# Performance work log

Measured on AMD Instinct MI355X. Metric: run time of the kernel, lower is better.

## Reference

```python
import jax, jax.numpy as jnp
import numpy as np

B, D, H, W, K = 2, 128, 256, 256, 4
OFFSET_SCALE = 1.0
BN_EPS = 1e-5


def conv2d(x, w, b=None, pad='SAME'):
    y = jax.lax.conv_general_dilated(x, w, (1, 1), pad,
                                     dimension_numbers=('NCHW', 'OIHW', 'NCHW'))
    if b is not None:
        y = y + b[None, :, None, None]
    return y


def grid_sample_border(img, gx, gy):
    # img: (b,d,H,W); gx,gy: (b,K,H,W) normalized coords in [-1,1]
    # bilinear, padding_mode='border', align_corners=True
    b, d, h, w = img.shape
    x = jnp.clip((gx + 1.0) * 0.5 * (w - 1), 0.0, w - 1)
    y = jnp.clip((gy + 1.0) * 0.5 * (h - 1), 0.0, h - 1)
    x0f = jnp.floor(x); y0f = jnp.floor(y)
    wx = x - x0f; wy = y - y0f
    x0 = x0f.astype(jnp.int32); y0 = y0f.astype(jnp.int32)
    x1 = jnp.minimum(x0 + 1, w - 1); y1 = jnp.minimum(y0 + 1, h - 1)
    imgT = jnp.transpose(img, (0, 2, 3, 1))  # (b,H,W,d)
    bidx = jnp.arange(b)[:, None, None, None]  # broadcasts over (b,K,H,W)
    def gather(yi, xi):
        return imgT[bidx, yi, xi]  # (b,K,H,W,d)
    out = (gather(y0, x0) * ((1 - wx) * (1 - wy))[..., None]
           + gather(y0, x1) * (wx * (1 - wy))[..., None]
           + gather(y1, x0) * ((1 - wx) * wy)[..., None]
           + gather(y1, x1) * (wx * wy)[..., None])
    return out  # (b,K,H,W,d)


def setup_inputs() -> dict:
    key = jax.random.key(0)
    ks = jax.random.split(key, 6)
    return {
        'bev': jax.random.normal(ks[0], (B, D, H, W), jnp.float32),
        'offset_w': jax.random.normal(ks[1], (2 * K, D, 3, 3), jnp.float32) * 0.02,
        'offset_b': jax.random.normal(ks[2], (2 * K,), jnp.float32) * 0.02,
        'weight_w': jax.random.normal(ks[3], (K, D, 3, 3), jnp.float32) * 0.05,
        'weight_b': jnp.zeros((K,), jnp.float32),
        'proj_w': jax.random.normal(ks[4], (D, D, 1, 1), jnp.float32) * (1.0 / np.sqrt(D)),
        'bn_gamma': jnp.ones((D,), jnp.float32),
        'bn_beta': jnp.zeros((D,), jnp.float32),
    }


def reference(bev, offset_w, offset_b, weight_w, weight_b, proj_w, bn_gamma, bn_beta):
    b, d, h, w = bev.shape
    # per-pixel K offsets (pixels) and K attention weights
    offsets = conv2d(bev, offset_w, offset_b) * OFFSET_SCALE  # (b,2K,H,W)
    w_logits = conv2d(bev, weight_w, weight_b)                # (b,K,H,W)
    attn = jax.nn.softmax(w_logits, axis=1)                   # softmax over K
    # base grid: replicates torch meshgrid(xy) + transpose (requires H==W)
    xs = jnp.linspace(-1.0, 1.0, w)
    ys = jnp.linspace(-1.0, 1.0, h)
    base_x = xs[:, None] * jnp.ones((1, h), jnp.float32)  # base_x[i,j] = xs[i]
    base_y = jnp.ones((w, 1), jnp.float32) * ys[None, :]  # base_y[i,j] = ys[j]
    off = offsets.reshape(b, K, 2, h, w)
    dx = off[:, :, 0]  # (b,K,H,W)
    dy = off[:, :, 1]
    dx_n = dx * (2.0 / (w - 1)) if w > 1 else dx * 0.0
    dy_n = dy * (2.0 / (h - 1)) if h > 1 else dy * 0.0
    gx = base_x[None, None] + dx_n  # (b,K,H,W)
    gy = base_y[None, None] + dy_n
    sampled = grid_sample_border(bev, gx, gy)  # (b,K,H,W,d)
    aggregated = jnp.einsum('bkhwd,bkhw->bdhw', sampled, attn)
    # proj: 1x1 conv (no bias) + BatchNorm2d (training mode: batch stats) + GELU(exact)
    y = conv2d(aggregated, proj_w)
    mean = jnp.mean(y, axis=(0, 2, 3), keepdims=True)
    var = jnp.mean((y - mean) ** 2, axis=(0, 2, 3), keepdims=True)
    y = (y - mean) * jax.lax.rsqrt(var + BN_EPS)
    y = y * bn_gamma[None, :, None, None] + bn_beta[None, :, None, None]
    return jax.nn.gelu(y, approximate=False)
```

## Files before the change

### kernel.cpp

```cpp
#include <hip/hip_runtime.h>
#include <math.h>

#define BB 2
#define DD 128
#define HH 256
#define WW 256
#define KK 4
#define HWC (HH*WW)
#define SROW2 320

typedef unsigned int u32;
typedef unsigned short ushort;
typedef __attribute__((ext_vector_type(8))) short bf16x8;
typedef __attribute__((ext_vector_type(4))) float f32x4;

#define OA_OFF    0
#define WTT_OFF   1572864
#define WP_OFF    1589248
#define STATS_OFF 1603072
#define PART_OFF  1603392
#define BEVT_OFF  1605440
#define YBF_OFF   9994048
#define PACC_OFF  18382656
#define PART2_OFF PACC_OFF
#define WBF_OFF   26771264
#define WCB_OFF   26779456
#define WS_NEED_BEVT  ((size_t)PACC_OFF * 4)
#define WS_NEED_FULL3 ((size_t)(WCB_OFF + 9216) * 4)

__device__ __forceinline__ u32 f2bf(float x) {
    u32 u = __builtin_bit_cast(u32, x);
    return (u + 0x7fffu + ((u >> 16) & 1u)) >> 16;
}
__device__ __forceinline__ u32 pkbf(float a, float b) {
    return f2bf(a) | (f2bf(b) << 16);
}
__device__ __forceinline__ float bflo(u32 d) { return __builtin_bit_cast(float, d << 16); }
__device__ __forceinline__ float bfhi(u32 d) { return __builtin_bit_cast(float, d & 0xffff0000u); }

__global__ __launch_bounds__(256) void k0_prep(
    const float* __restrict__ projw, const float* __restrict__ offw,
    const float* __restrict__ wtw, float* __restrict__ wtT, float* __restrict__ wp)
{
    int idx = blockIdx.x * 256 + threadIdx.x;
    if (idx < 16384) {
        int d = idx >> 7, o = idx & 127;
        wtT[d * 128 + o] = projw[o * 128 + d];
    }
    if (idx < 13824) {
        int c = idx / 108; int r = idx % 108; int o = r / 9; int t = r % 9;
        wp[idx] = (o < 8) ? offw[(o*128 + c)*9 + t] : wtw[((o-8)*128 + c)*9 + t];
    }
}

__global__ __launch_bounds__(256) void k0bc(
    const float* __restrict__ projw, const float* __restrict__ offw,
    const float* __restrict__ wtw, ushort* __restrict__ wbf,
    ushort* __restrict__ wcb)
{
    int idx = blockIdx.x * 256 + threadIdx.x;
    if (idx < 16384) wbf[idx] = (ushort)f2bf(projw[idx]);
    if (idx < 18432) {
        int tap = idx >> 11;
        int rem = idx & 2047;
        int oo = rem >> 7, c = rem & 127;
        float v = 0.f;
        if (oo < 8)       v = offw[(oo*128 + c)*9 + tap];
        else if (oo < 12) v = wtw[((oo-8)*128 + c)*9 + tap];
        wcb[idx] = (ushort)f2bf(v);
    }
}

__global__ __launch_bounds__(256) void k2t_bf(
    const float* __restrict__ bev, ushort* __restrict__ bevtb)
{
    __shared__ float T[64 * 128];
    int tid = threadIdx.x;
    int bidx = blockIdx.x;
    int b = bidx >> 10;
    int rem = bidx & 1023;
    int yrow = rem >> 2;
    int x0 = (rem & 3) << 6;

    const float* src = bev + ((size_t)b * DD) * HWC + (size_t)yrow * WW + x0;
    #pragma unroll 4
    for (int k = 0; k < 32; k++) {
        int flat = k * 256 + tid;
        int d = flat >> 6, xl = flat & 63;
        float v = src[(size_t)d * HWC + xl];
        T[xl * 128 + (((d >> 2) ^ (xl & 31)) << 2) + (d & 3)] = v;
    }
    __syncthreads();
    ushort* dst = bevtb + (((size_t)b * HH + yrow) * WW + x0) * 128;
    #pragma unroll 4
    for (int k = 0; k < 8; k++) {
        int flat = k * 256 + tid;
        int d4 = flat & 31, xl = (flat >> 5) & 63;
        float4 v = *(const float4*)&T[xl * 128 + ((d4 ^ (xl & 31)) << 2)];
        uint2 pk;
        pk.x = pkbf(v.x, v.y);
        pk.y = pkbf(v.z, v.w);
        *(uint2*)(dst + (size_t)xl * 128 + (d4 << 2)) = pk;
    }
}

__global__ __launch_bounds__(256) void k1m_conv_mfma(
    const ushort* __restrict__ bevtb, const ushort* __restrict__ wcb,
    const float* __restrict__ offb, const float* __restrict__ wtb,
    float* __restrict__ oa)
{
    __shared__ uint4 lds4[3168];

    int tid = threadIdx.x;
    int wv = tid >> 6;
    int l = tid & 63;
    int lm = l & 15, lk = l >> 4;
    int wgid = blockIdx.x;
    int lin = (wgid & 7) * 256 + (wgid >> 3);
    int b = lin >> 10;
    int i = (lin >> 2) & 255;
    int jt = lin & 3;
    int x0 = jt * 64;

    const ushort* bb = bevtb + (size_t)b * HWC * 128;
    for (int z = tid; z < 3168; z += 256) {
        int row = z / 1056;
        int rem = z - row * 1056;
        int pl = rem >> 4;
        int q  = rem & 15;
        int yy = i - 1 + row;
        int x  = x0 - 1 + pl;
        bool ok = ((unsigned)yy < HH) && ((unsigned)x < WW);
        uint4 v = make_uint4(0u, 0u, 0u, 0u);
        if (ok) v = *(const uint4*)(bb + ((size_t)(yy * WW + x) << 7) + q * 8);
        lds4[row * 1056 + pl * 16 + (q ^ (pl & 15))] = v;
    }
    __syncthreads();

    f32x4 acc = (f32x4)(0.f);
    #pragma unroll
    for (int dy = 0; dy < 3; dy++) {
        #pragma unroll
        for (int dx = 0; dx < 3; dx++) {
            int pl = wv * 16 + lm + dx;
            const uint4* bp = &lds4[dy * 1056 + pl * 16];
            int sx = pl & 15;
            const ushort* ap = wcb + (size_t)((dy*3 + dx) * 16 + lm) * 128 + lk * 8;
            #pragma unroll
            for (int kk = 0; kk < 4; kk++) {
                bf16x8 bfr = *(const bf16x8*)&bp[(kk*4 + lk) ^ sx];
                bf16x8 afr = *(const bf16x8*)(ap + kk * 32);
                acc = __builtin_amdgcn_mfma_f32_16x16x32_bf16(afr, bfr, acc, 0, 0, 0);
            }
        }
    }

    float v[4];
    #pragma unroll
    for (int r = 0; r < 4; r++) v[r] = acc[r];

    int j = x0 + wv * 16 + lm;
    if (lk < 2) {
        #pragma unroll
        for (int r = 0; r < 4; r++) v[r] += offb[lk*4 + r];
    } else if (lk == 2) {
        float l4[4];
        #pragma unroll
        for (int r = 0; r < 4; r++) l4[r] = v[r] + wtb[r];
        float m = fmaxf(fmaxf(l4[0], l4[1]), fmaxf(l4[2], l4[3]));
        float e[4]; float se = 0.f;
        #pragma unroll
        for (int r = 0; r < 4; r++) { e[r] = expf(l4[r] - m); se += e[r]; }
        float inv = 1.f / se;
        #pragma unroll
        for (int r = 0; r < 4; r++) v[r] = e[r] * inv;
    }
    if (lk < 3) {
        size_t basep = (size_t)b * 12 * HWC + (size_t)i * WW + j;
        #pragma unroll
        for (int r = 0; r < 4; r++)
            oa[basep + (size_t)(lk*4 + r) * HWC] = v[r];
    }
}

#define TAPPTR(t) (bt + ((size_t)((((t) & 1) ? (pa[(t) >> 1] >> 16) : (pa[(t) >> 1] & 0xffffu))) << 7))
#define FMA8(S, V, W) do { \
    S[0] = fmaf(W, bflo((V).x), S[0]); S[1] = fmaf(W, bfhi((V).x), S[1]); \
    S[2] = fmaf(W, bflo((V).y), S[2]); S[3] = fmaf(W, bfhi((V).y), S[3]); \
    S[4] = fmaf(W, bflo((V).z), S[4]); S[5] = fmaf(W, bfhi((V).z), S[5]); \
    S[6] = fmaf(W, bflo((V).w), S[6]); S[7] = fmaf(W, bfhi((V).w), S[7]); \
} while (0)

__global__ __launch_bounds__(256, 4) void k2f_sample_proj(
    const ushort* __restrict__ bevtb, const float* __restrict__ oa,
    const ushort* __restrict__ wbf, ushort* __restrict__ ybf,
    float* __restrict__ part2)
{
    __shared__ uint4 P[32 * 16];

    int tid = threadIdx.x;
    int wgid = blockIdx.x;
    int lin = (wgid & 7) * 512 + (wgid >> 3);
    int b = lin >> 11;
    int pix0 = (lin & 2047) << 5;

    int q8 = tid & 7;
    int pixl = tid >> 3;
    int pix = pix0 + pixl;
    int p = pix >> 8;
    int q = pix & 255;

    const float* ob = oa + (size_t)b * 12 * HWC + (size_t)p * WW + q;
    unsigned pa[8]; float cw[16];
    #pragma unroll
    for (int k = 0; k < 4; k++) {
        float dx = ob[(size_t)(2*k)   * HWC];
        float dy = ob[(size_t)(2*k+1) * HWC];
        float a  = ob[(size_t)(8+k)   * HWC];
        float x  = fminf(fmaxf((float)p + dx, 0.f), (float)(WW-1));
        float yv = fminf(fmaxf((float)q + dy, 0.f), (float)(HH-1));
        float x0f = floorf(x); float y0f = floorf(yv);
        int x0 = (int)x0f; int y0 = (int)y0f;
        int x1 = min(x0 + 1, WW - 1); int y1 = min(y0 + 1, HH - 1);
        float wx = x - x0f; float wy = yv - y0f;
        pa[k*2+0] = (unsigned)(y0*WW + x0) | ((unsigned)(y0*WW + x1) << 16);
        pa[k*2+1] = (unsigned)(y1*WW + x0) | ((unsigned)(y1*WW + x1) << 16);
        cw[k*4+0] = a * (1.f - wx) * (1.f - wy);
        cw[k*4+1] = a * wx * (1.f - wy);
        cw[k*4+2] = a * (1.f - wx) * wy;
        cw[k*4+3] = a * wx * wy;
    }

    const ushort* bt = bevtb + (size_t)b * HWC * 128 + q8 * 8;

    float s[2][8];
    #pragma unroll
    for (int c = 0; c < 2; c++)
        #pragma unroll
        for (int e = 0; e < 8; e++) s[c][e] = 0.f;

    uint4 L0[8], L1[8];
    #pragma unroll
    for (int t = 0; t < 8; t++) L0[t] = *(const uint4*)(TAPPTR(t));
    #pragma unroll
    for (int t = 0; t < 8; t++) L1[t] = *(const uint4*)(TAPPTR(t + 8));
    #pragma unroll
    for (int t = 0; t < 8; t++) {
        uint4 v = L0[t];
        L0[t] = *(const uint4*)(TAPPTR(t) + 64);
        FMA8(s[0], v, cw[t]);
    }
    #pragma unroll
    for (int t = 0; t < 8; t++) {
        uint4 v = L1[t];
        L1[t] = *(const uint4*)(TAPPTR(t + 8) + 64);
        FMA8(s[0], v, cw[t + 8]);
    }
    #pragma unroll
    for (int t = 0; t < 8; t++) FMA8(s[1], L0[t], cw[t]);
    #pragma unroll
    for (int t = 0; t < 8; t++) FMA8(s[1], L1[t], cw[t + 8]);

    int sxr = pixl & 15;
    #pragma unroll
    for (int c = 0; c < 2; c++) {
        uint4 pk;
        pk.x = pkbf(s[c][0], s[c][1]);
        pk.y = pkbf(s[c][2], s[c][3]);
        pk.z = pkbf(s[c][4], s[c][5]);
        pk.w = pkbf(s[c][6], s[c][7]);
        P[pixl * 16 + ((c * 8 + q8) ^ sxr)] = pk;
    }
    __syncthreads();

    int wv = tid >> 6;
    int l = tid & 63;
    int lm = l & 15, lk = l >> 4;
    int o0 = wv << 5;

    f32x4 acc[2][2];
    #pragma unroll
    for (int ot = 0; ot < 2; ot++)
        #pragma unroll
        for (int nt = 0; nt < 2; nt++)
            acc[ot][nt] = (f32x4)(0.f);

    #pragma unroll
    for (int ot = 0; ot < 2; ot++) {
        const ushort* ap = wbf + (size_t)(o0 + ot * 16 + lm) * 128 + lk * 8;
        bf16x8 a4[4];
        #pragma unroll
        for (int kk = 0; kk < 4; kk++)
            a4[kk] = *(const bf16x8*)(ap + kk * 32);
        #pragma unroll
        for (int nt = 0; nt < 2; nt++) {
            int row = nt * 16 + lm;
            #pragma unroll
            for (int kk = 0; kk < 4; kk++) {
                bf16x8 bfr = *(const bf16x8*)&P[row * 16 + ((kk * 4 + lk) ^ lm)];
                acc[ot][nt] = __builtin_amdgcn_mfma_f32_16x16x32_bf16(
                    a4[kk], bfr, acc[ot][nt], 0, 0, 0);
            }
        }
    }

    #pragma unroll
    for (int ot = 0; ot < 2; ot++)
        #pragma unroll
        for (int nt = 0; nt < 2; nt++)
            #pragma unroll
            for (int r = 0; r < 4; r++)
                ybf[((size_t)b * DD + o0 + ot * 16 + lk * 4 + r) * HWC + pix0 + nt * 16 + lm]
                    = (ushort)f2bf(acc[ot][nt][r]);

    float sm[2][4], sq[2][4];
    #pragma unroll
    for (int ot = 0; ot < 2; ot++)
        #pragma unroll
        for (int r = 0; r < 4; r++) { sm[ot][r] = 0.f; sq[ot][r] = 0.f; }
    #pragma unroll
    for (int ot = 0; ot < 2; ot++)
        #pragma unroll
        for (int nt = 0; nt < 2; nt++)
            #pragma unroll
            for (int r = 0; r < 4; r++) {
                float v = acc[ot][nt][r];
                sm[ot][r] += v;
                sq[ot][r] = fmaf(v, v, sq[ot][r]);
            }
    #pragma unroll
    for (int m = 1; m < 16; m <<= 1) {
        #pragma unroll
        for (int ot = 0; ot < 2; ot++)
            #pragma unroll
            for (int r = 0; r < 4; r++) {
                sm[ot][r] += __shfl_xor(sm[ot][r], m);
                sq[ot][r] += __shfl_xor(sq[ot][r], m);
            }
    }
    if (lm == 0) {
        float* pw = part2 + (size_t)wgid * 256;
        #pragma unroll
        for (int ot = 0; ot < 2; ot++)
            #pragma unroll
            for (int r = 0; r < 4; r++) {
                int o = o0 + ot * 16 + lk * 4 + r;
                pw[o] = sm[ot][r];
                pw[128 + o] = sq[ot][r];
            }
    }
}

__global__ __launch_bounds__(256) void k3b_finalize2(
    const float* __restrict__ part2, const float* __restrict__ gamma,
    const float* __restrict__ beta, float* __restrict__ stats)
{
    int o = blockIdx.x; int tid = threadIdx.x;
    double s = 0.0, s2 = 0.0;
    for (int w = tid; w < 4096; w += 256) {
        s  += (double)part2[(size_t)w * 256 + o];
        s2 += (double)part2[(size_t)w * 256 + 128 + o];
    }
    __shared__ double ls[256], ls2[256];
    ls[tid] = s; ls2[tid] = s2;
    __syncthreads();
    for (int off = 128; off > 0; off >>= 1) {
        if (tid < off) { ls[tid] += ls[tid+off]; ls2[tid] += ls2[tid+off]; }
        __syncthreads();
    }
    if (tid == 0) {
        double N = (double)(BB * HWC);
        double mean = ls[0] / N;
        double var = ls2[0] / N - mean * mean;
        double invs = 1.0 / sqrt(var + 1e-5);
        double g = (double)gamma[o];
        stats[o*2]   = (float)(g * invs);
        stats[o*2+1] = (float)((double)beta[o] - mean * g * invs);
    }
}

__global__ __launch_bounds__(256) void k4_bn_gelu_bf(
    const ushort* __restrict__ ybf, const float* __restrict__ stats,
    float* __restrict__ out)
{
    size_t idx8 = (size_t)blockIdx.x * 256 + threadIdx.x;
    uint4 v = ((const uint4*)ybf)[idx8];
    int o = (int)((idx8 * 8) / HWC) % DD;
    float sc = stats[o*2], sh = stats[o*2+1];
    const float is2 = 0.70710678118654752f;
    float g[8];
    g[0] = fmaf(bflo(v.x), sc, sh); g[1] = fmaf(bfhi(v.x), sc, sh);
    g[2] = fmaf(bflo(v.y), sc, sh); g[3] = fmaf(bfhi(v.y), sc, sh);
    g[4] = fmaf(bflo(v.z), sc, sh); g[5] = fmaf(bfhi(v.z), sc, sh);
    g[6] = fmaf(bflo(v.w), sc, sh); g[7] = fmaf(bfhi(v.w), sc, sh);
    float4 o0, o1;
    o0.x = 0.5f * g[0] * (1.f + erff(g[0] * is2));
    o0.y = 0.5f * g[1] * (1.f + erff(g[1] * is2));
    o0.z = 0.5f * g[2] * (1.f + erff(g[2] * is2));
    o0.w = 0.5f * g[3] * (1.f + erff(g[3] * is2));
    o1.x = 0.5f * g[4] * (1.f + erff(g[4] * is2));
    o1.y = 0.5f * g[5] * (1.f + erff(g[5] * is2));
    o1.z = 0.5f * g[6] * (1.f + erff(g[6] * is2));
    o1.w = 0.5f * g[7] * (1.f + erff(g[7] * is2));
    ((float4*)out)[idx8 * 2]     = o0;
    ((float4*)out)[idx8 * 2 + 1] = o1;
}

__global__ __launch_bounds__(256) void k1_convs(
    const float* __restrict__ bev, const float* __restrict__ wp,
    const float* __restrict__ offb, const float* __restrict__ wtb,
    float* __restrict__ oa)
{
    __shared__ float rows[2][3][260];
    int tid = threadIdx.x;
    int p = blockIdx.x;
    int b = p / HH; int i = p % HH; int j = tid;
    const float* bb = bev + (size_t)b * DD * HWC;

    if (tid < 12) { int bf = tid / 6, r = tid % 6; rows[bf][r >> 1][(r & 1) ? 257 : 0] = 0.f; }
    #pragma unroll
    for (int l = 0; l < 3; l++) {
        int yy = i + l - 1;
        rows[0][l][1 + tid] = ((unsigned)yy < HH) ? bb[yy * WW + tid] : 0.f;
    }
    __syncthreads();

    float acc[12];
    #pragma unroll
    for (int o = 0; o < 12; o++) acc[o] = 0.f;

    for (int c = 0; c < 128; c++) {
        int cb = c & 1, nb = cb ^ 1;
        float rv[3];
        if (c < 127) {
            const float* pln = bb + (size_t)(c + 1) * HWC;
            #pragma unroll
            for (int l = 0; l < 3; l++) {
                int yy = i + l - 1;
                rv[l] = ((unsigned)yy < HH) ? pln[yy * WW + tid] : 0.f;
            }
        }
        float v[9];
        #pragma unroll
        for (int dy = 0; dy < 3; dy++)
            #pragma unroll
            for (int dx = 0; dx < 3; dx++)
                v[dy*3 + dx] = rows[cb][dy][tid + dx];
        const float* wc = wp + c * 108;
        #pragma unroll
        for (int o = 0; o < 12; o++) {
            float s = acc[o];
            #pragma unroll
            for (int t = 0; t < 9; t++) s = fmaf(wc[o*9 + t], v[t], s);
            acc[o] = s;
        }
        if (c < 127) {
            #pragma unroll
            for (int l = 0; l < 3; l++) rows[nb][l][1 + tid] = rv[l];
        }
        __syncthreads();
    }

    float outv[12];
    #pragma unroll
    for (int o = 0; o < 8; o++) outv[o] = acc[o] + offb[o];
    float l4[4];
    #pragma unroll
    for (int k = 0; k < 4; k++) l4[k] = acc[8+k] + wtb[k];
    float m = fmaxf(fmaxf(l4[0], l4[1]), fmaxf(l4[2], l4[3]));
    float e[4]; float se = 0.f;
    #pragma unroll
    for (int k = 0; k < 4; k++) { e[k] = expf(l4[k] - m); se += e[k]; }
    float inv = 1.f / se;
    #pragma unroll
    for (int k = 0; k < 4; k++) outv[8+k] = e[k] * inv;

    size_t basep = (size_t)b * 12 * HWC + (size_t)i * WW + j;
    #pragma unroll
    for (int o = 0; o < 12; o++) oa[basep + (size_t)o * HWC] = outv[o];
}

__global__ __launch_bounds__(512, 2) void k2_sample_proj(
    const float* __restrict__ bev, const float* __restrict__ oa,
    const float* __restrict__ wt, float* __restrict__ y)
{
    __shared__ float S[2][16 * SROW2];
    int tid = threadIdx.x;
    int bidx = blockIdx.x;
    int b  = bidx >> 8;
    int p0 = ((bidx >> 4) & 15) * 16;
    int q0 = (bidx & 15) * 16;
    int pix = tid & 255;
    int gq = pix >> 4;
    int gp = pix & 15;
    int dgrp = tid >> 8;
    int swr = gp * 20 + gq;
    int wv = tid >> 6;
    int wvu = __builtin_amdgcn_readfirstlane(wv);
    int lane = tid & 63;
    int lp = lane >> 2;
    int q4 = (lane & 3) << 2;
    int soff = lp * 20 + q4;

    const float* ob = oa + (size_t)b * 12 * HWC + (size_t)(p0 + gp) * WW + (q0 + gq);
    unsigned pa[8]; float cw[16];
    #pragma unroll
    for (int k = 0; k < 4; k++) {
        float dx = ob[(size_t)(2*k)   * HWC];
        float dy = ob[(size_t)(2*k+1) * HWC];
        float a  = ob[(size_t)(8+k)   * HWC];
        float x  = fminf(fmaxf((float)(p0 + gp) + dx, 0.f), (float)(WW-1));
        float yv = fminf(fmaxf((float)(q0 + gq) + dy, 0.f), (float)(HH-1));
        float x0f = floorf(x); float y0f = floorf(yv);
        int x0 = (int)x0f; int y0 = (int)y0f;
        int x1 = min(x0 + 1, WW - 1); int y1 = min(y0 + 1, HH - 1);
        float wx = x - x0f; float wy = yv - y0f;
        pa[k*2+0] = (unsigned)(y0*WW + x0) | ((unsigned)(y0*WW + x1) << 16);
        pa[k*2+1] = (unsigned)(y1*WW + x0) | ((unsigned)(y1*WW + x1) << 16);
        cw[k*4+0] = a * (1.f - wx) * (1.f - wy);
        cw[k*4+1] = a * wx * (1.f - wy);
        cw[k*4+2] = a * (1.f - wx) * wy;
        cw[k*4+3] = a * wx * wy;
    }
    const float* bb = bev + (size_t)b * DD * HWC;
    float acc[64];
    #pragma unroll
    for (int t = 0; t < 64; t++) acc[t] = 0.f;
    #pragma unroll
    for (int dd = 0; dd < 8; dd++) {
        const float* pl = bb + (size_t)(dgrp*8 + dd) * HWC;
        float s = 0.f;
        #pragma unroll
        for (int t = 0; t < 8; t++) {
            unsigned a01 = pa[t];
            s = fmaf(cw[2*t],   pl[a01 & 0xffffu], s);
            s = fmaf(cw[2*t+1], pl[a01 >> 16], s);
        }
        S[0][(dgrp*8 + dd) * SROW2 + swr] = s;
    }
    __syncthreads();
    for (int c = 0; c < 8; c++) {
        int cur = c & 1;
        const float* Sc = &S[cur][0];
        float* Sn = &S[cur ^ 1][0];
        int d0 = c * 16;
        int d0n = d0 + 16;
        bool more = (c < 7);
        #pragma unroll
        for (int dl = 0; dl < 16; dl++) {
            if (dl < 8) {
                if (more) {
                    const float* pl = bb + (size_t)(d0n + dgrp*8 + dl) * HWC;
                    float s = 0.f;
                    #pragma unroll
                    for (int t = 0; t < 8; t++) {
                        unsigned a01 = pa[t];
                        s = fmaf(cw[2*t],   pl[a01 & 0xffffu], s);
                        s = fmaf(cw[2*t+1], pl[a01 >> 16], s);
                    }
                    Sn[(dgrp*8 + dl) * SROW2 + swr] = s;
                }
            }
            float4 sv = *(const float4*)(Sc + dl * SROW2 + soff);
            const float4* wq = (const float4*)(wt + (size_t)(d0 + dl) * 128 + wvu * 16);
            #pragma unroll
            for (int oi4 = 0; oi4 < 4; oi4++) {
                float4 w4 = wq[oi4];
                int ob4 = oi4 * 16;
                acc[ob4+ 0] = fmaf(w4.x, sv.x, acc[ob4+ 0]);
                acc[ob4+ 1] = fmaf(w4.x, sv.y, acc[ob4+ 1]);
                acc[ob4+ 2] = fmaf(w4.x, sv.z, acc[ob4+ 2]);
                acc[ob4+ 3] = fmaf(w4.x, sv.w, acc[ob4+ 3]);
                acc[ob4+ 4] = fmaf(w4.y, sv.x, acc[ob4+ 4]);
                acc[ob4+ 5] = fmaf(w4.y, sv.y, acc[ob4+ 5]);
                acc[ob4+ 6] = fmaf(w4.y, sv.z, acc[ob4+ 6]);
                acc[ob4+ 7] = fmaf(w4.y, sv.w, acc[ob4+ 7]);
                acc[ob4+ 8] = fmaf(w4.z, sv.x, acc[ob4+ 8]);
                acc[ob4+ 9] = fmaf(w4.z, sv.y, acc[ob4+ 9]);
                acc[ob4+10] = fmaf(w4.z, sv.z, acc[ob4+10]);
                acc[ob4+11] = fmaf(w4.z, sv.w, acc[ob4+11]);
                acc[ob4+12] = fmaf(w4.w, sv.x, acc[ob4+12]);
                acc[ob4+13] = fmaf(w4.w, sv.y, acc[ob4+13]);
                acc[ob4+14] = fmaf(w4.w, sv.z, acc[ob4+14]);
                acc[ob4+15] = fmaf(w4.w, sv.w, acc[ob4+15]);
            }
        }
        __syncthreads();
    }
    size_t base = (size_t)b * DD * HWC + (size_t)(p0 + lp) * WW + (q0 + q4);
    #pragma unroll
    for (int oi = 0; oi < 16; oi++) {
        int o = wv * 16 + oi;
        float4 v = make_float4(acc[oi*4+0], acc[oi*4+1], acc[oi*4+2], acc[oi*4+3]);
        *(float4*)(y + base + (size_t)o * HWC) = v;
    }
}

__global__ __launch_bounds__(256) void k3_partial(
    const float* __restrict__ y, double* __restrict__ part)
{
    int blk = blockIdx.x;
    int o = blk >> 2; int sub = blk & 3; int b = sub >> 1; int half = sub & 1;
    const float4* pl = (const float4*)(y + ((size_t)b * DD + o) * HWC + half * (HWC/2));
    int tid = threadIdx.x;
    double s = 0.0, s2 = 0.0;
    for (int idx = tid; idx < HWC/8; idx += 256) {
        float4 v = pl[idx];
        s  += (double)v.x + (double)v.y + (double)v.z + (double)v.w;
        s2 += (double)v.x*v.x + (double)v.y*v.y + (double)v.z*v.z + (double)v.w*v.w;
    }
    __shared__ double ls[256], ls2[256];
    ls[tid] = s; ls2[tid] = s2;
    __syncthreads();
    for (int off = 128; off > 0; off >>= 1) {
        if (tid < off) { ls[tid] += ls[tid+off]; ls2[tid] += ls2[tid+off]; }
        __syncthreads();
    }
    if (tid == 0) { part[blk*2] = ls[0]; part[blk*2+1] = ls2[0]; }
}

__global__ __launch_bounds__(128) void k3_finalize(
    const double* __restrict__ part, const float* __restrict__ gamma,
    const float* __restrict__ beta, float* __restrict__ stats)
{
    int o = threadIdx.x;
    double s = 0.0, s2 = 0.0;
    #pragma unroll
    for (int j = 0; j < 4; j++) { s += part[(o*4+j)*2]; s2 += part[(o*4+j)*2+1]; }
    double N = (double)(BB * HWC);
    double mean = s / N;
    double var = s2 / N - mean * mean;
    double invs = 1.0 / sqrt(var + 1e-5);
    double g = (double)gamma[o];
    stats[o*2]   = (float)(g * invs);
    stats[o*2+1] = (float)((double)beta[o] - mean * g * invs);
}

__global__ __launch_bounds__(256) void k4_bn_gelu(
    float* __restrict__ y, const float* __restrict__ stats)
{
    size_t idx4 = (size_t)blockIdx.x * 256 + threadIdx.x;
    float4* p = (float4*)y;
    float4 v = p[idx4];
    int o = (int)((idx4 * 4) / HWC) % DD;
    float sc = stats[o*2], sh = stats[o*2+1];
    const float inv_sqrt2 = 0.70710678118654752f;
    float g0 = fmaf(v.x, sc, sh);
    float g1 = fmaf(v.y, sc, sh);
    float g2 = fmaf(v.z, sc, sh);
    float g3 = fmaf(v.w, sc, sh);
    v.x = 0.5f * g0 * (1.f + erff(g0 * inv_sqrt2));
    v.y = 0.5f * g1 * (1.f + erff(g1 * inv_sqrt2));
    v.z = 0.5f * g2 * (1.f + erff(g2 * inv_sqrt2));
    v.w = 0.5f * g3 * (1.f + erff(g3 * inv_sqrt2));
    p[idx4] = v;
}

extern "C" void kernel_launch(void* const* d_in, const int* in_sizes, int n_in,
                              void* d_out, int out_size, void* d_ws, size_t ws_size,
                              hipStream_t stream) {
    const float* bev   = (const float*)d_in[0];
    const float* offw  = (const float*)d_in[1];
    const float* offb  = (const float*)d_in[2];
    const float* wtw   = (const float*)d_in[3];
    const float* wtb   = (const float*)d_in[4];
    const float* projw = (const float*)d_in[5];
    const float* gamma = (const float*)d_in[6];
    const float* beta  = (const float*)d_in[7];
    float* out = (float*)d_out;
    float* wsf = (float*)d_ws;

    float* oa    = wsf + OA_OFF;
    float* wtT   = wsf + WTT_OFF;
    float* wp    = wsf + WP_OFF;
    float* stats = wsf + STATS_OFF;
    double* part = (double*)(wsf + PART_OFF);
    ushort* bevtb = (ushort*)(wsf + BEVT_OFF);
    ushort* ybf   = (ushort*)(wsf + YBF_OFF);
    ushort* wbf  = (ushort*)(wsf + WBF_OFF);
    ushort* wcb  = (ushort*)(wsf + WCB_OFF);
    float* part2 = wsf + PART2_OFF;

    bool full3 = ws_size >= WS_NEED_FULL3;

    if (full3) {
        hipLaunchKernelGGL(k0bc, dim3(72), dim3(256), 0, stream,
                           projw, offw, wtw, wbf, wcb);
        hipLaunchKernelGGL(k2t_bf, dim3(2048), dim3(256), 0, stream, bev, bevtb);
        hipLaunchKernelGGL(k1m_conv_mfma, dim3(2048), dim3(256), 0, stream,
                           bevtb, wcb, offb, wtb, oa);
        hipLaunchKernelGGL(k2f_sample_proj, dim3(4096), dim3(256), 0, stream,
                           bevtb, oa, wbf, ybf, part2);
        hipLaunchKernelGGL(k3b_finalize2, dim3(128), dim3(256), 0, stream,
                           part2, gamma, beta, stats);
        hipLaunchKernelGGL(k4_bn_gelu_bf, dim3((BB*DD*HWC)/2048), dim3(256), 0, stream,
                           ybf, stats, out);
    } else {
        hipLaunchKernelGGL(k0_prep, dim3(64), dim3(256), 0, stream,
                           projw, offw, wtw, wtT, wp);
        hipLaunchKernelGGL(k1_convs, dim3(BB*HH), dim3(256), 0, stream,
                           bev, wp, offb, wtb, oa);
        hipLaunchKernelGGL(k2_sample_proj, dim3(BB*256), dim3(512), 0, stream,
                           bev, oa, wtT, out);
        hipLaunchKernelGGL(k3_partial, dim3(512), dim3(256), 0, stream, out, part);
        hipLaunchKernelGGL(k3_finalize, dim3(1), dim3(128), 0, stream,
                           part, gamma, beta, stats);
        hipLaunchKernelGGL(k4_bn_gelu, dim3((BB*DD*HWC)/1024), dim3(256), 0, stream,
                           out, stats);
    }
}
```

Baseline: 151.3 us.

## Process four output rows per conv block with rolling three-row LDS buffer

```diff
diff --git a/kernel.cpp b/kernel.cpp
--- a/kernel.cpp
+++ b/kernel.cpp
@@ -109,78 +109,100 @@
     const float* __restrict__ offb, const float* __restrict__ wtb,
     float* __restrict__ oa)
 {
-    __shared__ uint4 lds4[3168];
+    __shared__ uint4 lds4[3 * 1056];
 
     int tid = threadIdx.x;
     int wv = tid >> 6;
     int l = tid & 63;
     int lm = l & 15, lk = l >> 4;
     int wgid = blockIdx.x;
-    int lin = (wgid & 7) * 256 + (wgid >> 3);
-    int b = lin >> 10;
-    int i = (lin >> 2) & 255;
+    int lin = (wgid & 7) * 64 + (wgid >> 3);
+    int b = lin >> 8;
+    int band = (lin >> 2) & 63;
     int jt = lin & 3;
+    int i0 = band * 4;
     int x0 = jt * 64;
 
     const ushort* bb = bevtb + (size_t)b * HWC * 128;
-    for (int z = tid; z < 3168; z += 256) {
-        int row = z / 1056;
-        int rem = z - row * 1056;
-        int pl = rem >> 4;
-        int q  = rem & 15;
-        int yy = i - 1 + row;
-        int x  = x0 - 1 + pl;
-        bool ok = ((unsigned)yy < HH) && ((unsigned)x < WW);
-        uint4 v = make_uint4(0u, 0u, 0u, 0u);
-        if (ok) v = *(const uint4*)(bb + ((size_t)(yy * WW + x) << 7) + q * 8);
-        lds4[row * 1056 + pl * 16 + (q ^ (pl & 15))] = v;
-    }
+
+    #define STAGE_ROW(a, s) do {                                                  \
+        int _a = (a); int _s = (s);                                               \
+        bool rok = ((unsigned)_a < HH);                                           \
+        for (int z = tid; z < 1056; z += 256) {                                   \
+            int pl = z >> 4; int qq = z & 15;                                     \
+            int x = x0 - 1 + pl;                                                  \
+            bool ok = rok && ((unsigned)x < WW);                                  \
+            uint4 v = make_uint4(0u, 0u, 0u, 0u);                                 \
+            if (ok) v = *(const uint4*)(bb + ((size_t)(_a * WW + x) << 7) + qq * 8); \
+            lds4[_s * 1056 + pl * 16 + (qq ^ (pl & 15))] = v;                     \
+        }                                                                         \
+    } while (0)
+
+    STAGE_ROW(i0 - 1, i0 % 3);
+    STAGE_ROW(i0,     (i0 + 1) % 3);
+    STAGE_ROW(i0 + 1, (i0 + 2) % 3);
     __syncthreads();
 
-    f32x4 acc = (f32x4)(0.f);
-    #pragma unroll
-    for (int dy = 0; dy < 3; dy++) {
-        #pragma unroll
-        for (int dx = 0; dx < 3; dx++) {
-            int pl = wv * 16 + lm + dx;
-            const uint4* bp = &lds4[dy * 1056 + pl * 16];
-            int sx = pl & 15;
-            const ushort* ap = wcb + (size_t)((dy*3 + dx) * 16 + lm) * 128 + lk * 8;
-            #pragma unroll
-            for (int kk = 0; kk < 4; kk++) {
-                bf16x8 bfr = *(const bf16x8*)&bp[(kk*4 + lk) ^ sx];
-                bf16x8 afr = *(const bf16x8*)(ap + kk * 32);
-                acc = __builtin_amdgcn_mfma_f32_16x16x32_bf16(afr, bfr, acc, 0, 0, 0);
+    #pragma unroll
+    for (int r = 0; r < 4; r++) {
+        int i = i0 + r;
+        int s0 = i % 3;
+        int s1 = (i + 1) % 3;
+        int s2 = (i + 2) % 3;
+        int slots[3] = { s0, s1, s2 };
+
+        f32x4 acc = (f32x4)(0.f);
+        #pragma unroll
+        for (int dy = 0; dy < 3; dy++) {
+            #pragma unroll
+            for (int dx = 0; dx < 3; dx++) {
+                int pl = wv * 16 + lm + dx;
+                const uint4* bp = &lds4[slots[dy] * 1056 + pl * 16];
+                int sx = pl & 15;
+                const ushort* ap = wcb + (size_t)((dy*3 + dx) * 16 + lm) * 128 + lk * 8;
+                #pragma unroll
+                for (int kk = 0; kk < 4; kk++) {
+                    bf16x8 bfr = *(const bf16x8*)&bp[(kk*4 + lk) ^ sx];
+                    bf16x8 afr = *(const bf16x8*)(ap + kk * 32);
+                    acc = __builtin_amdgcn_mfma_f32_16x16x32_bf16(afr, bfr, acc, 0, 0, 0);
+                }
             }
         }
-    }
-
-    float v[4];
-    #pragma unroll
-    for (int r = 0; r < 4; r++) v[r] = acc[r];
-
-    int j = x0 + wv * 16 + lm;
-    if (lk < 2) {
-        #pragma unroll
-        for (int r = 0; r < 4; r++) v[r] += offb[lk*4 + r];
-    } else if (lk == 2) {
-        float l4[4];
-        #pragma unroll
-        for (int r = 0; r < 4; r++) l4[r] = v[r] + wtb[r];
-        float m = fmaxf(fmaxf(l4[0], l4[1]), fmaxf(l4[2], l4[3]));
-        float e[4]; float se = 0.f;
-        #pragma unroll
-        for (int r = 0; r < 4; r++) { e[r] = expf(l4[r] - m); se += e[r]; }
-        float inv = 1.f / se;
-        #pragma unroll
-        for (int r = 0; r < 4; r++) v[r] = e[r] * inv;
-    }
-    if (lk < 3) {
-        size_t basep = (size_t)b * 12 * HWC + (size_t)i * WW + j;
-        #pragma unroll
-        for (int r = 0; r < 4; r++)
-            oa[basep + (size_t)(lk*4 + r) * HWC] = v[r];
-    }
+
+        float v[4];
+        #pragma unroll
+        for (int t = 0; t < 4; t++) v[t] = acc[t];
+
+        int j = x0 + wv * 16 + lm;
+        if (lk < 2) {
+            #pragma unroll
+            for (int t = 0; t < 4; t++) v[t] += offb[lk*4 + t];
+        } else if (lk == 2) {
+            float l4[4];
+            #pragma unroll
+            for (int t = 0; t < 4; t++) l4[t] = v[t] + wtb[t];
+            float m = fmaxf(fmaxf(l4[0], l4[1]), fmaxf(l4[2], l4[3]));
+            float e[4]; float se = 0.f;
+            #pragma unroll
+            for (int t = 0; t < 4; t++) { e[t] = expf(l4[t] - m); se += e[t]; }
+            float inv = 1.f / se;
+            #pragma unroll
+            for (int t = 0; t < 4; t++) v[t] = e[t] * inv;
+        }
+        if (lk < 3) {
+            size_t basep = (size_t)b * 12 * HWC + (size_t)i * WW + j;
+            #pragma unroll
+            for (int t = 0; t < 4; t++)
+                oa[basep + (size_t)(lk*4 + t) * HWC] = v[t];
+        }
+
+        __syncthreads();
+        if (r < 3) {
+            STAGE_ROW(i + 2, i % 3);
+            __syncthreads();
+        }
+    }
+    #undef STAGE_ROW
 }
 
 #define TAPPTR(t) (bt + ((size_t)((((t) & 1) ? (pa[(t) >> 1] >> 16) : (pa[(t) >> 1] & 0xffffu))) << 7))
@@ -687,7 +709,7 @@
         hipLaunchKernelGGL(k0bc, dim3(72), dim3(256), 0, stream,
                            projw, offw, wtw, wbf, wcb);
         hipLaunchKernelGGL(k2t_bf, dim3(2048), dim3(256), 0, stream, bev, bevtb);
-        hipLaunchKernelGGL(k1m_conv_mfma, dim3(2048), dim3(256), 0, stream,
+        hipLaunchKernelGGL(k1m_conv_mfma, dim3(512), dim3(256), 0, stream,
                            bevtb, wcb, offb, wtb, oa);
         hipLaunchKernelGGL(k2f_sample_proj, dim3(4096), dim3(256), 0, stream,
                            bevtb, oa, wbf, ybf, part2);
```

Measured after the change: 140.0 us. 7.4% less time.
